# Optimization experiments

Measured on AMD Instinct MI355X. Metric: run time of the kernel, lower is better.

## Reference

```python
import jax, jax.numpy as jnp
import numpy as np

B, T, D, H, Q = 8, 1024, 256, 4, 3
DK = D // H


def _ln(x, g, b):
    m = x.mean(-1, keepdims=True)
    v = x.var(-1, keepdims=True)
    return (x - m) / jnp.sqrt(v + 1e-5) * g + b


def _grn(x, f1w, f1b, f2w, f2b, gw, gb, lng, lnb):
    # GatedResidualNetwork (input_size == output_size, dropout in eval mode)
    eta1 = jax.nn.elu(x @ f1w.T + f1b)
    eta2 = eta1 @ f2w.T + f2b
    a = jax.nn.sigmoid(eta2 @ gw.T + gb) * eta2
    return _ln(x + a, lng, lnb)


def setup_inputs() -> dict:
    key = jax.random.key(0)
    ks = jax.random.split(key, 24)
    s = 0.02
    p = {}
    p['x'] = jax.random.normal(ks[0], (B, T, D), dtype=jnp.float32)
    # GRN 1 (temporal enrichment before attention)
    p['g1_f1w'] = jax.random.normal(ks[1], (D, D)) * s
    p['g1_f1b'] = jnp.zeros((D,))
    p['g1_f2w'] = jax.random.normal(ks[2], (D, D)) * s
    p['g1_f2b'] = jnp.zeros((D,))
    p['g1_gw'] = jax.random.normal(ks[3], (D, D)) * s
    p['g1_gb'] = jnp.zeros((D,))
    p['g1_lng'] = jnp.ones((D,))
    p['g1_lnb'] = jnp.zeros((D,))
    # Multi-head self-attention
    p['wq'] = jax.random.normal(ks[4], (D, D)) * s
    p['wk'] = jax.random.normal(ks[5], (D, D)) * s
    p['wv'] = jax.random.normal(ks[6], (D, D)) * s
    p['wo_w'] = jax.random.normal(ks[7], (D, D)) * s
    p['wo_b'] = jnp.zeros((D,))
    p['attn_lng'] = jnp.ones((D,))
    p['attn_lnb'] = jnp.zeros((D,))
    # GRN 2 (post-attention gating)
    p['g2_f1w'] = jax.random.normal(ks[8], (D, D)) * s
    p['g2_f1b'] = jnp.zeros((D,))
    p['g2_f2w'] = jax.random.normal(ks[9], (D, D)) * s
    p['g2_f2b'] = jnp.zeros((D,))
    p['g2_gw'] = jax.random.normal(ks[10], (D, D)) * s
    p['g2_gb'] = jnp.zeros((D,))
    p['g2_lng'] = jnp.ones((D,))
    p['g2_lnb'] = jnp.zeros((D,))
    # Quantile heads: Linear(D -> Q)
    p['qh_w'] = jax.random.normal(ks[11], (Q, D)) * s
    p['qh_b'] = jnp.zeros((Q,))
    return p


def reference(x, g1_f1w, g1_f1b, g1_f2w, g1_f2b, g1_gw, g1_gb, g1_lng, g1_lnb,
              wq, wk, wv, wo_w, wo_b, attn_lng, attn_lnb,
              g2_f1w, g2_f1b, g2_f2w, g2_f2b, g2_gw, g2_gb, g2_lng, g2_lnb,
              qh_w, qh_b):
    b, t, d = x.shape
    h = _grn(x, g1_f1w, g1_f1b, g1_f2w, g1_f2b, g1_gw, g1_gb, g1_lng, g1_lnb)
    # self-attention (W_q/W_k/W_v have no bias, per module)
    q = (h @ wq.T).reshape(b, t, H, DK)
    k = (h @ wk.T).reshape(b, t, H, DK)
    v = (h @ wv.T).reshape(b, t, H, DK)
    scale = 1.0 / np.sqrt(DK).astype(np.float32)
    scores = jnp.einsum('bthd,bshd->bhts', q, k) * scale  # [B,H,T,T]
    attn = jax.nn.softmax(scores, axis=-1)
    ctx = jnp.einsum('bhts,bshd->bthd', attn, v).reshape(b, t, d)
    attn_out = ctx @ wo_w.T + wo_b
    h2 = _ln(h + attn_out, attn_lng, attn_lnb)
    h3 = _grn(h2, g2_f1w, g2_f1b, g2_f2w, g2_f2b, g2_gw, g2_gb, g2_lng, g2_lnb)
    # quantile heads on the last decoder step (CUDAQuantileHeadsFunction: [B,D]->[B,Q])
    out = h3[:, -1, :] @ qh_w.T + qh_b  # [B, Q]
    return out
```

## Files before the change

### kernel.cpp

```cpp
#include <hip/hip_runtime.h>
#include <hip/hip_bf16.h>
#include <math.h>

#define DD 256
#define BB 8
#define TT 1024
#define MM (BB*TT)
#define NH 4
#define DKH 64
#define NQ 3

typedef __attribute__((ext_vector_type(8))) short bf16x8;
typedef __attribute__((ext_vector_type(4))) float f32x4;
typedef unsigned short u16;
typedef unsigned int u32;

__device__ __forceinline__ float bf2f(u16 u) {
  return __uint_as_float(((u32)u) << 16);
}
__device__ __forceinline__ u16 f2bf(float x) {
  __hip_bfloat16 h = __float2bfloat16(x);
  return *reinterpret_cast<u16*>(&h);
}
__device__ __forceinline__ uint2 pack4(float a, float b, float c, float d) {
  uint2 r;
  r.x = (u32)f2bf(a) | ((u32)f2bf(b) << 16);
  r.y = (u32)f2bf(c) | ((u32)f2bf(d) << 16);
  return r;
}
__device__ __forceinline__ float wred(float v) {
#pragma unroll
  for (int off = 32; off; off >>= 1) v += __shfl_xor(v, off);
  return v;
}

template<bool ABF, int ACT>
__global__ __launch_bounds__(256) void gemm64(const void* __restrict__ A_,
                                              const float* __restrict__ W,
                                              const float* __restrict__ bias,
                                              u16* __restrict__ out)
{
  __shared__ u16 As[64][264];
  __shared__ u16 Bs[64][264];
  const int tid  = threadIdx.x;
  const int lane = tid & 63, wave = tid >> 6;
  const int wr = wave >> 1, wc = wave & 1;
  const int q  = lane >> 4, lr = lane & 15;
  const int m0 = blockIdx.x * 64, n0 = blockIdx.y * 64;

#pragma unroll
  for (int p = 0; p < 8; ++p) {
    const int c = tid + p * 256;
    const int row = c >> 5, col = (c & 31) * 8;
    if constexpr (ABF) {
      *(uint4*)&As[row][col] = *(const uint4*)((const u16*)A_ + (size_t)(m0 + row) * DD + col);
    } else {
      const float* ap = (const float*)A_ + (size_t)(m0 + row) * DD + col;
      const float4 v0 = *(const float4*)ap, v1 = *(const float4*)(ap + 4);
      *(uint2*)&As[row][col]     = pack4(v0.x, v0.y, v0.z, v0.w);
      *(uint2*)&As[row][col + 4] = pack4(v1.x, v1.y, v1.z, v1.w);
    }
    const float* wp = W + (size_t)(n0 + row) * DD + col;
    const float4 w0 = *(const float4*)wp, w1 = *(const float4*)(wp + 4);
    *(uint2*)&Bs[row][col]     = pack4(w0.x, w0.y, w0.z, w0.w);
    *(uint2*)&Bs[row][col + 4] = pack4(w1.x, w1.y, w1.z, w1.w);
  }
  __syncthreads();

  f32x4 acc[2][2] = {};
#pragma unroll
  for (int kk = 0; kk < 8; ++kk) {
    const int koff = kk * 32 + q * 8;
    bf16x8 av[2], bv[2];
    av[0] = *(const bf16x8*)&As[wr * 32 + lr][koff];
    av[1] = *(const bf16x8*)&As[wr * 32 + 16 + lr][koff];
    bv[0] = *(const bf16x8*)&Bs[wc * 32 + lr][koff];
    bv[1] = *(const bf16x8*)&Bs[wc * 32 + 16 + lr][koff];
#pragma unroll
    for (int i = 0; i < 2; ++i)
#pragma unroll
      for (int j = 0; j < 2; ++j)
        acc[i][j] = __builtin_amdgcn_mfma_f32_16x16x32_bf16(av[i], bv[j], acc[i][j], 0, 0, 0);
  }

#pragma unroll
  for (int i = 0; i < 2; ++i) {
#pragma unroll
    for (int j = 0; j < 2; ++j) {
      const int col = n0 + wc * 32 + j * 16 + lr;
      const float bvv = bias ? bias[col] : 0.f;
#pragma unroll
      for (int t = 0; t < 4; ++t) {
        const int row = m0 + wr * 32 + i * 16 + q * 4 + t;
        float v = acc[i][j][t] + bvv;
        if (ACT == 1) v = v > 0.f ? v : expm1f(v);
        out[(size_t)row * DD + col] = f2bf(v);
      }
    }
  }
}

__global__ __launch_bounds__(256) void gemm_kv(const u16* __restrict__ A_,
                                               const float* __restrict__ Wk,
                                               const float* __restrict__ Wv,
                                               u16* __restrict__ kout,
                                               u16* __restrict__ vout)
{
  __shared__ u16 As[64][264];
  __shared__ u16 Bs[64][264];
  const int tid  = threadIdx.x;
  const int lane = tid & 63, wave = tid >> 6;
  const int wr = wave >> 1, wc = wave & 1;
  const int q  = lane >> 4, lr = lane & 15;
  const int ny = blockIdx.y;
  const float* W = (ny < 4) ? Wk : Wv;
  u16* out = (ny < 4) ? kout : vout;
  const int m0 = blockIdx.x * 64, n0 = (ny & 3) * 64;

#pragma unroll
  for (int p = 0; p < 8; ++p) {
    const int c = tid + p * 256;
    const int row = c >> 5, col = (c & 31) * 8;
    *(uint4*)&As[row][col] = *(const uint4*)(A_ + (size_t)(m0 + row) * DD + col);
    const float* wp = W + (size_t)(n0 + row) * DD + col;
    const float4 w0 = *(const float4*)wp, w1 = *(const float4*)(wp + 4);
    *(uint2*)&Bs[row][col]     = pack4(w0.x, w0.y, w0.z, w0.w);
    *(uint2*)&Bs[row][col + 4] = pack4(w1.x, w1.y, w1.z, w1.w);
  }
  __syncthreads();

  f32x4 acc[2][2] = {};
#pragma unroll
  for (int kk = 0; kk < 8; ++kk) {
    const int koff = kk * 32 + q * 8;
    bf16x8 av[2], bv[2];
    av[0] = *(const bf16x8*)&As[wr * 32 + lr][koff];
    av[1] = *(const bf16x8*)&As[wr * 32 + 16 + lr][koff];
    bv[0] = *(const bf16x8*)&Bs[wc * 32 + lr][koff];
    bv[1] = *(const bf16x8*)&Bs[wc * 32 + 16 + lr][koff];
#pragma unroll
    for (int i = 0; i < 2; ++i)
#pragma unroll
      for (int j = 0; j < 2; ++j)
        acc[i][j] = __builtin_amdgcn_mfma_f32_16x16x32_bf16(av[i], bv[j], acc[i][j], 0, 0, 0);
  }

#pragma unroll
  for (int i = 0; i < 2; ++i) {
#pragma unroll
    for (int j = 0; j < 2; ++j) {
      const int col = n0 + wc * 32 + j * 16 + lr;
#pragma unroll
      for (int t = 0; t < 4; ++t) {
        const int row = m0 + wr * 32 + i * 16 + q * 4 + t;
        out[(size_t)row * DD + col] = f2bf(acc[i][j][t]);
      }
    }
  }
}

__global__ __launch_bounds__(256) void grn_gate_ln(
    const u16* __restrict__ eta2, const float* __restrict__ W,
    const float* __restrict__ gb, const float* __restrict__ x,
    const float* __restrict__ lng, const float* __restrict__ lnb,
    u16* __restrict__ hout, float* __restrict__ hlast)
{
  __shared__ u16 As[32][136];
  __shared__ u16 Bs[256][136];
  __shared__ float red_s[32][5];
  __shared__ float red_q[32][5];
  __shared__ float smean[32], srstd[32];

  const int tid  = threadIdx.x;
  const int lane = tid & 63, wave = tid >> 6;
  const int q  = lane >> 4, lr = lane & 15;
  const int m0 = blockIdx.x * 32;

  f32x4 acc[2][4] = {};

  for (int k0 = 0; k0 < DD; k0 += 128) {
#pragma unroll
    for (int p = 0; p < 2; ++p) {
      const int c = tid + p * 256;
      const int row = c >> 4, col = (c & 15) * 8;
      *(uint4*)&As[row][col] = *(const uint4*)(eta2 + (size_t)(m0 + row) * DD + k0 + col);
    }
#pragma unroll
    for (int p = 0; p < 16; ++p) {
      const int c = tid + p * 256;
      const int row = c >> 4, col = (c & 15) * 8;
      const float* wp = W + (size_t)row * DD + k0 + col;
      const float4 w0 = *(const float4*)wp, w1 = *(const float4*)(wp + 4);
      *(uint2*)&Bs[row][col]     = pack4(w0.x, w0.y, w0.z, w0.w);
      *(uint2*)&Bs[row][col + 4] = pack4(w1.x, w1.y, w1.z, w1.w);
    }
    __syncthreads();
#pragma unroll
    for (int kk = 0; kk < 4; ++kk) {
      const int koff = kk * 32 + q * 8;
      bf16x8 av[2], bv[4];
#pragma unroll
      for (int i = 0; i < 2; ++i) av[i] = *(const bf16x8*)&As[i * 16 + lr][koff];
#pragma unroll
      for (int j = 0; j < 4; ++j) bv[j] = *(const bf16x8*)&Bs[wave * 64 + j * 16 + lr][koff];
#pragma unroll
      for (int i = 0; i < 2; ++i)
#pragma unroll
        for (int j = 0; j < 4; ++j)
          acc[i][j] = __builtin_amdgcn_mfma_f32_16x16x32_bf16(av[i], bv[j], acc[i][j], 0, 0, 0);
    }
    __syncthreads();
  }

  float pre[2][4][4];
#pragma unroll
  for (int i = 0; i < 2; ++i) {
#pragma unroll
    for (int j = 0; j < 4; ++j) {
      const int n = wave * 64 + j * 16 + lr;
      const float gbn = gb[n];
#pragma unroll
      for (int t = 0; t < 4; ++t) {
        const int grow = m0 + i * 16 + q * 4 + t;
        const float gate = acc[i][j][t] + gbn;
        const float sig = 1.f / (1.f + expf(-gate));
        const float e2 = bf2f(eta2[(size_t)grow * DD + n]);
        pre[i][j][t] = x[(size_t)grow * DD + n] + sig * e2;
      }
    }
  }
#pragma unroll
  for (int i = 0; i < 2; ++i) {
#pragma unroll
    for (int t = 0; t < 4; ++t) {
      float s = 0.f, sq = 0.f;
#pragma unroll
      for (int j = 0; j < 4; ++j) { const float v = pre[i][j][t]; s += v; sq += v * v; }
#pragma unroll
      for (int m = 1; m <= 8; m <<= 1) { s += __shfl_xor(s, m); sq += __shfl_xor(sq, m); }
      if (lr == 0) {
        const int ml = i * 16 + q * 4 + t;
        red_s[ml][wave] = s;
        red_q[ml][wave] = sq;
      }
    }
  }
  __syncthreads();
  if (tid < 32) {
    const float s  = red_s[tid][0] + red_s[tid][1] + red_s[tid][2] + red_s[tid][3];
    const float sq = red_q[tid][0] + red_q[tid][1] + red_q[tid][2] + red_q[tid][3];
    const float mean = s * (1.f / DD);
    const float var = sq * (1.f / DD) - mean * mean;
    smean[tid] = mean;
    srstd[tid] = rsqrtf(var + 1e-5f);
  }
  __syncthreads();
#pragma unroll
  for (int i = 0; i < 2; ++i) {
#pragma unroll
    for (int j = 0; j < 4; ++j) {
      const int n = wave * 64 + j * 16 + lr;
      const float gn = lng[n], bn = lnb[n];
#pragma unroll
      for (int t = 0; t < 4; ++t) {
        const int ml = i * 16 + q * 4 + t;
        const int grow = m0 + ml;
        const float hn = (pre[i][j][t] - smean[ml]) * srstd[ml] * gn + bn;
        hout[(size_t)grow * DD + n] = f2bf(hn);
        if ((grow & (TT - 1)) == (TT - 1))
          hlast[(size_t)(grow >> 10) * DD + n] = hn;
      }
    }
  }
}

__global__ __launch_bounds__(256) void qk_softmax_ctx(
    const float* __restrict__ hlast, const u16* __restrict__ kbuf,
    const u16* __restrict__ vbuf, const float* __restrict__ wq,
    const float* __restrict__ wow, const float* __restrict__ f1w,
    const float* __restrict__ f2w, const float* __restrict__ gw,
    u16* __restrict__ wbf, float* __restrict__ ctxbuf)
{
  __shared__ float hl[DD], qh[DKH];
  __shared__ float red[8];
  __shared__ float pr[TT];
  __shared__ float part[8][DKH];
  const int h = blockIdx.x, b = blockIdx.y;
  const int tid = threadIdx.x, lane = tid & 63, w = tid >> 6;

  {
    const int bid = b * NH + h;
    const int mi = bid >> 3;
    const float* src = (mi == 0) ? wow : (mi == 1) ? f1w : (mi == 2) ? f2w : gw;
    const int off = (bid & 7) * 8192 + tid * 32;
    const float* sp = src + off;
    u16* dp = wbf + mi * 65536 + off;
#pragma unroll
    for (int i = 0; i < 32; i += 4) {
      const float4 v = *(const float4*)(sp + i);
      *(uint2*)(dp + i) = pack4(v.x, v.y, v.z, v.w);
    }
  }

  hl[tid] = hlast[(size_t)b * DD + tid];
  __syncthreads();
  {
    const int j = tid >> 2, seg = tid & 3;
    const float* wr = wq + (size_t)(h * DKH + j) * DD + seg * 64;
    const float* sp = hl + seg * 64;
    float acc = 0.f;
#pragma unroll
    for (int k = 0; k < 64; k += 4) {
      const float4 w4 = *(const float4*)(wr + k);
      acc += w4.x * sp[k] + w4.y * sp[k + 1] + w4.z * sp[k + 2] + w4.w * sp[k + 3];
    }
    acc += __shfl_xor(acc, 1);
    acc += __shfl_xor(acc, 2);
    if (seg == 0) qh[j] = acc;
  }
  __syncthreads();

  float sv[4], mx = -3.0e38f;
#pragma unroll
  for (int i = 0; i < 4; ++i) {
    const int s = tid + 256 * i;
    const u16* kr = kbuf + ((size_t)(b * TT + s)) * DD + h * DKH;
    float acc = 0.f;
#pragma unroll
    for (int d = 0; d < DKH; d += 8) {
      const bf16x8 kv = *(const bf16x8*)(kr + d);
#pragma unroll
      for (int e = 0; e < 8; ++e) acc += bf2f((u16)kv[e]) * qh[d + e];
    }
    sv[i] = acc * 0.125f;
    mx = fmaxf(mx, sv[i]);
  }
#pragma unroll
  for (int off = 32; off; off >>= 1) mx = fmaxf(mx, __shfl_xor(mx, off));
  if (lane == 0) red[w] = mx;
  __syncthreads();
  mx = fmaxf(fmaxf(red[0], red[1]), fmaxf(red[2], red[3]));
  float sum = 0.f;
#pragma unroll
  for (int i = 0; i < 4; ++i) { sv[i] = expf(sv[i] - mx); sum += sv[i]; }
  sum = wred(sum);
  if (lane == 0) red[4 + w] = sum;
  __syncthreads();
  const float inv = 1.f / (red[4] + red[5] + red[6] + red[7]);
#pragma unroll
  for (int i = 0; i < 4; ++i) pr[tid + 256 * i] = sv[i] * inv;
  __syncthreads();

  {
    const int np = (tid & 31) * 2, sg = tid >> 5;
    const u16* vp = vbuf + ((size_t)(b * TT + sg * 128)) * DD + h * DKH + np;
    const float* pp = pr + sg * 128;
    float a0 = 0.f, a1 = 0.f;
    for (int s = 0; s < 128; ++s) {
      const u32 vv = *(const u32*)(vp + (size_t)s * DD);
      const float p = pp[s];
      a0 += p * bf2f((u16)(vv & 0xffffu));
      a1 += p * bf2f((u16)(vv >> 16));
    }
    part[sg][np] = a0; part[sg][np + 1] = a1;
  }
  __syncthreads();
  if (tid < DKH) {
    float s = 0.f;
#pragma unroll
    for (int g = 0; g < 8; ++g) s += part[g][tid];
    ctxbuf[(size_t)b * DD + h * DKH + tid] = s;
  }
}

__device__ __forceinline__ void mv256b(const u16* __restrict__ W16,
                                       const float* __restrict__ srcbuf,
                                       float* __restrict__ dst,
                                       int wave, int lane)
{
  const int half = lane >> 5, l32 = lane & 31;
  float s[8];
  {
    const float4 s0 = *(const float4*)(srcbuf + l32 * 8);
    const float4 s1 = *(const float4*)(srcbuf + l32 * 8 + 4);
    s[0] = s0.x; s[1] = s0.y; s[2] = s0.z; s[3] = s0.w;
    s[4] = s1.x; s[5] = s1.y; s[6] = s1.z; s[7] = s1.w;
  }
#pragma unroll
  for (int i = 0; i < 8; ++i) {
    const int r = wave * 16 + i * 2 + half;
    const bf16x8 wv = *(const bf16x8*)(W16 + (size_t)r * DD + l32 * 8);
    float acc = 0.f;
#pragma unroll
    for (int e = 0; e < 8; ++e) acc += bf2f((u16)wv[e]) * s[e];
#pragma unroll
    for (int off = 16; off; off >>= 1) acc += __shfl_xor(acc, off);
    if (l32 == 0) dst[r] = acc;
  }
}

#define LN_STEP(val, gam, bet, dst) \
  __syncthreads(); \
  if (tid < DD) { lnS[tid] = (val); lnQ[tid] = (val) * (val); } \
  __syncthreads(); \
  if (tid < 64) { \
    float s_ = 0.f, q_ = 0.f; \
    _Pragma("unroll") \
    for (int i_ = 0; i_ < 4; ++i_) { s_ += lnS[tid + 64 * i_]; q_ += lnQ[tid + 64 * i_]; } \
    s_ = wred(s_); q_ = wred(q_); \
    if (tid == 0) { const float m_ = s_ * (1.f / DD); red2[0] = m_; red2[1] = rsqrtf(q_ * (1.f / DD) - m_ * m_ + 1e-5f); } \
  } \
  __syncthreads(); \
  if (tid < DD) dst[tid] = ((val) - red2[0]) * red2[1] * gam[tid] + bet[tid]; \
  __syncthreads();

__global__ __launch_bounds__(1024) void tail2(
    const float* __restrict__ hlast, const float* __restrict__ ctxbuf,
    const u16* __restrict__ wbf,
    const float* __restrict__ wob, const float* __restrict__ alng, const float* __restrict__ alnb,
    const float* __restrict__ f1b, const float* __restrict__ f2b,
    const float* __restrict__ gbv, const float* __restrict__ lng, const float* __restrict__ lnb,
    const float* __restrict__ qhw, const float* __restrict__ qhb,
    float* __restrict__ out)
{
  __shared__ float hl[DD], bufA[DD], bufB[DD], bufC[DD], part0[DD];
  __shared__ float lnS[DD], lnQ[DD];
  __shared__ float red2[2];
  const int b = blockIdx.x, tid = threadIdx.x;
  const int wave = tid >> 6, lane = tid & 63;

  if (tid < DD) {
    hl[tid]   = hlast[(size_t)b * DD + tid];
    bufB[tid] = ctxbuf[(size_t)b * DD + tid];
  }
  __syncthreads();

  mv256b(wbf + 0 * 65536, bufB, part0, wave, lane);
  __syncthreads();
  float v = 0.f;
  if (tid < DD) v = hl[tid] + part0[tid] + wob[tid];
  LN_STEP(v, alng, alnb, bufA)

  mv256b(wbf + 1 * 65536, bufA, part0, wave, lane);
  __syncthreads();
  if (tid < DD) {
    const float e1 = part0[tid] + f1b[tid];
    bufB[tid] = e1 > 0.f ? e1 : expm1f(e1);
  }
  __syncthreads();

  mv256b(wbf + 2 * 65536, bufB, part0, wave, lane);
  __syncthreads();
  if (tid < DD) bufC[tid] = part0[tid] + f2b[tid];
  __syncthreads();

  mv256b(wbf + 3 * 65536, bufC, part0, wave, lane);
  __syncthreads();
  v = 0.f;
  if (tid < DD) {
    const float g = part0[tid] + gbv[tid];
    v = bufA[tid] + (1.f / (1.f + expf(-g))) * bufC[tid];
  }
  LN_STEP(v, lng, lnb, bufA)

  if (tid < 64 * NQ) {
    const int qi = tid >> 6, l = tid & 63;
    float acc = 0.f;
#pragma unroll
    for (int i = 0; i < 4; ++i) acc += qhw[(size_t)qi * DD + l + 64 * i] * bufA[l + 64 * i];
    acc = wred(acc);
    if (l == 0) out[b * NQ + qi] = acc + qhb[qi];
  }
}

extern "C" void kernel_launch(void* const* d_in, const int* in_sizes, int n_in,
                              void* d_out, int out_size, void* d_ws, size_t ws_size,
                              hipStream_t stream)
{
  const float* x       = (const float*)d_in[0];
  const float* g1_f1w  = (const float*)d_in[1];
  const float* g1_f1b  = (const float*)d_in[2];
  const float* g1_f2w  = (const float*)d_in[3];
  const float* g1_f2b  = (const float*)d_in[4];
  const float* g1_gw   = (const float*)d_in[5];
  const float* g1_gb   = (const float*)d_in[6];
  const float* g1_lng  = (const float*)d_in[7];
  const float* g1_lnb  = (const float*)d_in[8];
  const float* wq      = (const float*)d_in[9];
  const float* wk      = (const float*)d_in[10];
  const float* wv      = (const float*)d_in[11];
  const float* wo_w    = (const float*)d_in[12];
  const float* wo_b    = (const float*)d_in[13];
  const float* attn_lng= (const float*)d_in[14];
  const float* attn_lnb= (const float*)d_in[15];
  const float* g2_f1w  = (const float*)d_in[16];
  const float* g2_f1b  = (const float*)d_in[17];
  const float* g2_f2w  = (const float*)d_in[18];
  const float* g2_f2b  = (const float*)d_in[19];
  const float* g2_gw   = (const float*)d_in[20];
  const float* g2_gb   = (const float*)d_in[21];
  const float* g2_lng  = (const float*)d_in[22];
  const float* g2_lnb  = (const float*)d_in[23];
  const float* qh_w    = (const float*)d_in[24];
  const float* qh_b    = (const float*)d_in[25];
  float* out = (float*)d_out;

  char* w8 = (char*)d_ws;
  u16*  eta1  = (u16*)(w8);
  u16*  wbf   = (u16*)(w8);
  u16*  eta2  = (u16*)(w8 + ((size_t)4  << 20));
  u16*  hbuf  = (u16*)(w8 + ((size_t)8  << 20));
  u16*  kbuf  = (u16*)(w8 + ((size_t)12 << 20));
  u16*  vbuf  = (u16*)(w8 + ((size_t)16 << 20));
  float* hlast = (float*)(w8 + ((size_t)20 << 20));
  float* ctxbuf = (float*)(w8 + ((size_t)20 << 20) + (64 << 10));

  const dim3 blk(256);
  const dim3 g1(MM / 64, DD / 64);

  gemm64<false, 1><<<g1, blk, 0, stream>>>((const void*)x,    g1_f1w, g1_f1b, eta1);
  gemm64<true,  0><<<g1, blk, 0, stream>>>((const void*)eta1, g1_f2w, g1_f2b, eta2);
  grn_gate_ln<<<dim3(MM / 32), blk, 0, stream>>>(eta2, g1_gw, g1_gb, x, g1_lng, g1_lnb, hbuf, hlast);
  gemm_kv<<<dim3(MM / 64, 8), blk, 0, stream>>>(hbuf, wk, wv, kbuf, vbuf);
  qk_softmax_ctx<<<dim3(NH, BB), blk, 0, stream>>>(hlast, kbuf, vbuf, wq,
                                                   wo_w, g2_f1w, g2_f2w, g2_gw,
                                                   wbf, ctxbuf);
  tail2<<<dim3(BB), dim3(1024), 0, stream>>>(hlast, ctxbuf, wbf,
                                             wo_b, attn_lng, attn_lnb,
                                             g2_f1b, g2_f2b, g2_gb, g2_lng, g2_lnb,
                                             qh_w, qh_b, out);
}
```

Before: 77.19 us.

## Precast input and all weights to bf16 in a dedicated kernel before GEMMs

Adds a precast kernel that converts x and nine weight matrices to bf16 once, so GEMM kernels load bf16 tiles directly instead of converting fp32 per block. This removes repeated weight conversions across the many GEMM blocks and the conversion work inside qk_softmax_ctx. In exchange it adds an extra kernel launch and a full read of x in fp32 plus a bf16 write and reread, which adds memory traffic.

Measured after the change: 77.32 us. Within noise of the previous version (+0.2%).

```diff
diff --git a/kernel.cpp b/kernel.cpp
--- a/kernel.cpp
+++ b/kernel.cpp
@@ -34,9 +34,48 @@
   return v;
 }
 
-template<bool ABF, int ACT>
-__global__ __launch_bounds__(256) void gemm64(const void* __restrict__ A_,
-                                              const float* __restrict__ W,
+#define NX8 (MM * DD / 8)
+#define NW8 (65536 / 8)
+#define NCHUNK (NX8 + 9 * NW8)
+
+__global__ __launch_bounds__(256) void precast(
+    const float* __restrict__ x,
+    const float* __restrict__ w0, const float* __restrict__ w1,
+    const float* __restrict__ w2, const float* __restrict__ w3,
+    const float* __restrict__ w4, const float* __restrict__ w5,
+    const float* __restrict__ w6, const float* __restrict__ w7,
+    const float* __restrict__ w8_, u16* __restrict__ wb,
+    u16* __restrict__ xb)
+{
+  const int c = blockIdx.x * 256 + threadIdx.x;
+  if (c >= NCHUNK) return;
+  const float* src;
+  u16* dst;
+  int off;
+  if (c < NX8) {
+    src = x; dst = xb; off = c * 8;
+  } else {
+    const int r = c - NX8;
+    const int mi = r / NW8;
+    off = (r - mi * NW8) * 8;
+    switch (mi) {
+      case 0: src = w0; break; case 1: src = w1; break;
+      case 2: src = w2; break; case 3: src = w3; break;
+      case 4: src = w4; break; case 5: src = w5; break;
+      case 6: src = w6; break; case 7: src = w7; break;
+      default: src = w8_; break;
+    }
+    dst = wb + mi * 65536;
+  }
+  const float4 v0 = *(const float4*)(src + off);
+  const float4 v1 = *(const float4*)(src + off + 4);
+  *(uint2*)(dst + off)     = pack4(v0.x, v0.y, v0.z, v0.w);
+  *(uint2*)(dst + off + 4) = pack4(v1.x, v1.y, v1.z, v1.w);
+}
+
+template<int ACT>
+__global__ __launch_bounds__(256) void gemm64(const u16* __restrict__ A_,
+                                              const u16* __restrict__ W,
                                               const float* __restrict__ bias,
                                               u16* __restrict__ out)
 {
@@ -52,18 +91,8 @@
   for (int p = 0; p < 8; ++p) {
     const int c = tid + p * 256;
     const int row = c >> 5, col = (c & 31) * 8;
-    if constexpr (ABF) {
-      *(uint4*)&As[row][col] = *(const uint4*)((const u16*)A_ + (size_t)(m0 + row) * DD + col);
-    } else {
-      const float* ap = (const float*)A_ + (size_t)(m0 + row) * DD + col;
-      const float4 v0 = *(const float4*)ap, v1 = *(const float4*)(ap + 4);
-      *(uint2*)&As[row][col]     = pack4(v0.x, v0.y, v0.z, v0.w);
-      *(uint2*)&As[row][col + 4] = pack4(v1.x, v1.y, v1.z, v1.w);
-    }
-    const float* wp = W + (size_t)(n0 + row) * DD + col;
-    const float4 w0 = *(const float4*)wp, w1 = *(const float4*)(wp + 4);
-    *(uint2*)&Bs[row][col]     = pack4(w0.x, w0.y, w0.z, w0.w);
-    *(uint2*)&Bs[row][col + 4] = pack4(w1.x, w1.y, w1.z, w1.w);
+    *(uint4*)&As[row][col] = *(const uint4*)(A_ + (size_t)(m0 + row) * DD + col);
+    *(uint4*)&Bs[row][col] = *(const uint4*)(W  + (size_t)(n0 + row) * DD + col);
   }
   __syncthreads();
 
@@ -101,8 +130,8 @@
 }
 
 __global__ __launch_bounds__(256) void gemm_kv(const u16* __restrict__ A_,
-                                               const float* __restrict__ Wk,
-                                               const float* __restrict__ Wv,
+                                               const u16* __restrict__ Wk,
+                                               const u16* __restrict__ Wv,
                                                u16* __restrict__ kout,
                                                u16* __restrict__ vout)
 {
@@ -113,7 +142,7 @@
   const int wr = wave >> 1, wc = wave & 1;
   const int q  = lane >> 4, lr = lane & 15;
   const int ny = blockIdx.y;
-  const float* W = (ny < 4) ? Wk : Wv;
+  const u16* W = (ny < 4) ? Wk : Wv;
   u16* out = (ny < 4) ? kout : vout;
   const int m0 = blockIdx.x * 64, n0 = (ny & 3) * 64;
 
@@ -122,10 +151,7 @@
     const int c = tid + p * 256;
     const int row = c >> 5, col = (c & 31) * 8;
     *(uint4*)&As[row][col] = *(const uint4*)(A_ + (size_t)(m0 + row) * DD + col);
-    const float* wp = W + (size_t)(n0 + row) * DD + col;
-    const float4 w0 = *(const float4*)wp, w1 = *(const float4*)(wp + 4);
-    *(uint2*)&Bs[row][col]     = pack4(w0.x, w0.y, w0.z, w0.w);
-    *(uint2*)&Bs[row][col + 4] = pack4(w1.x, w1.y, w1.z, w1.w);
+    *(uint4*)&Bs[row][col] = *(const uint4*)(W  + (size_t)(n0 + row) * DD + col);
   }
   __syncthreads();
 
@@ -160,7 +186,7 @@
 }
 
 __global__ __launch_bounds__(256) void grn_gate_ln(
-    const u16* __restrict__ eta2, const float* __restrict__ W,
+    const u16* __restrict__ eta2, const u16* __restrict__ W,
     const float* __restrict__ gb, const float* __restrict__ x,
     const float* __restrict__ lng, const float* __restrict__ lnb,
     u16* __restrict__ hout, float* __restrict__ hlast)
@@ -189,10 +215,7 @@
     for (int p = 0; p < 16; ++p) {
       const int c = tid + p * 256;
       const int row = c >> 4, col = (c & 15) * 8;
-      const float* wp = W + (size_t)row * DD + k0 + col;
-      const float4 w0 = *(const float4*)wp, w1 = *(const float4*)(wp + 4);
-      *(uint2*)&Bs[row][col]     = pack4(w0.x, w0.y, w0.z, w0.w);
-      *(uint2*)&Bs[row][col + 4] = pack4(w1.x, w1.y, w1.z, w1.w);
+      *(uint4*)&Bs[row][col] = *(const uint4*)(W + (size_t)row * DD + k0 + col);
     }
     __syncthreads();
 #pragma unroll
@@ -277,9 +300,7 @@
 __global__ __launch_bounds__(256) void qk_softmax_ctx(
     const float* __restrict__ hlast, const u16* __restrict__ kbuf,
     const u16* __restrict__ vbuf, const float* __restrict__ wq,
-    const float* __restrict__ wow, const float* __restrict__ f1w,
-    const float* __restrict__ f2w, const float* __restrict__ gw,
-    u16* __restrict__ wbf, float* __restrict__ ctxbuf)
+    float* __restrict__ ctxbuf)
 {
   __shared__ float hl[DD], qh[DKH];
   __shared__ float red[8];
@@ -287,20 +308,6 @@
   __shared__ float part[8][DKH];
   const int h = blockIdx.x, b = blockIdx.y;
   const int tid = threadIdx.x, lane = tid & 63, w = tid >> 6;
-
-  {
-    const int bid = b * NH + h;
-    const int mi = bid >> 3;
-    const float* src = (mi == 0) ? wow : (mi == 1) ? f1w : (mi == 2) ? f2w : gw;
-    const int off = (bid & 7) * 8192 + tid * 32;
-    const float* sp = src + off;
-    u16* dp = wbf + mi * 65536 + off;
-#pragma unroll
-    for (int i = 0; i < 32; i += 4) {
-      const float4 v = *(const float4*)(sp + i);
-      *(uint2*)(dp + i) = pack4(v.x, v.y, v.z, v.w);
-    }
-  }
 
   hl[tid] = hlast[(size_t)b * DD + tid];
   __syncthreads();
@@ -506,26 +513,29 @@
   float* out = (float*)d_out;
 
   char* w8 = (char*)d_ws;
-  u16*  eta1  = (u16*)(w8);
-  u16*  wbf   = (u16*)(w8);
-  u16*  eta2  = (u16*)(w8 + ((size_t)4  << 20));
-  u16*  hbuf  = (u16*)(w8 + ((size_t)8  << 20));
-  u16*  kbuf  = (u16*)(w8 + ((size_t)12 << 20));
-  u16*  vbuf  = (u16*)(w8 + ((size_t)16 << 20));
-  float* hlast = (float*)(w8 + ((size_t)20 << 20));
-  float* ctxbuf = (float*)(w8 + ((size_t)20 << 20) + (64 << 10));
+  u16*  wb    = (u16*)(w8);
+  u16*  xb    = (u16*)(w8 + ((size_t)2  << 20));
+  u16*  eta1  = (u16*)(w8 + ((size_t)6  << 20));
+  u16*  eta2  = (u16*)(w8 + ((size_t)10 << 20));
+  u16*  hbuf  = (u16*)(w8 + ((size_t)14 << 20));
+  u16*  kbuf  = (u16*)(w8 + ((size_t)18 << 20));
+  u16*  vbuf  = (u16*)(w8 + ((size_t)22 << 20));
+  float* hlast = (float*)(w8 + ((size_t)26 << 20));
+  float* ctxbuf = (float*)(w8 + ((size_t)26 << 20) + (64 << 10));
 
   const dim3 blk(256);
   const dim3 g1(MM / 64, DD / 64);
 
-  gemm64<false, 1><<<g1, blk, 0, stream>>>((const void*)x,    g1_f1w, g1_f1b, eta1);
-  gemm64<true,  0><<<g1, blk, 0, stream>>>((const void*)eta1, g1_f2w, g1_f2b, eta2);
-  grn_gate_ln<<<dim3(MM / 32), blk, 0, stream>>>(eta2, g1_gw, g1_gb, x, g1_lng, g1_lnb, hbuf, hlast);
-  gemm_kv<<<dim3(MM / 64, 8), blk, 0, stream>>>(hbuf, wk, wv, kbuf, vbuf);
-  qk_softmax_ctx<<<dim3(NH, BB), blk, 0, stream>>>(hlast, kbuf, vbuf, wq,
-                                                   wo_w, g2_f1w, g2_f2w, g2_gw,
-                                                   wbf, ctxbuf);
-  tail2<<<dim3(BB), dim3(1024), 0, stream>>>(hlast, ctxbuf, wbf,
+  precast<<<dim3((NCHUNK + 255) / 256), blk, 0, stream>>>(
+      x, g1_f1w, g1_f2w, g1_gw, wk, wv, wo_w, g2_f1w, g2_f2w, g2_gw, wb, xb);
+  gemm64<1><<<g1, blk, 0, stream>>>(xb,   wb + 0 * 65536, g1_f1b, eta1);
+  gemm64<0><<<g1, blk, 0, stream>>>(eta1, wb + 1 * 65536, g1_f2b, eta2);
+  grn_gate_ln<<<dim3(MM / 32), blk, 0, stream>>>(eta2, wb + 2 * 65536, g1_gb, x,
+                                                 g1_lng, g1_lnb, hbuf, hlast);
+  gemm_kv<<<dim3(MM / 64, 8), blk, 0, stream>>>(hbuf, wb + 3 * 65536, wb + 4 * 65536,
+                                                kbuf, vbuf);
+  qk_softmax_ctx<<<dim3(NH, BB), blk, 0, stream>>>(hlast, kbuf, vbuf, wq, ctxbuf);
+  tail2<<<dim3(BB), dim3(1024), 0, stream>>>(hlast, ctxbuf, wb + 5 * 65536,
                                              wo_b, attn_lng, attn_lnb,
                                              g2_f1b, g2_f2b, g2_gb, g2_lng, g2_lnb,
                                              qh_w, qh_b, out);
```

## Fold K/V projections into query-side vectors and split attention over sequence chunks

Applied to the files above, without the earlier changes.

Drops the full K and V GEMMs over all 8192 rows. The last-step query is projected back through Wk, so scores come straight from dot products with h. Unnormalised exp-weighted sums of h are built in 16 chunks per batch, then reduced in the tail and projected through Wv once. This removes the large K/V GEMM and its intermediate buffers and spreads attention over more blocks. In exchange, softmax no longer subtracts a max and instead clamps scores to ±30, which could lose accuracy for large scores.

Measured after the change: 89.60 us. +16.1%, slower.

```diff
diff --git a/kernel.cpp b/kernel.cpp
--- a/kernel.cpp
+++ b/kernel.cpp
@@ -9,6 +9,8 @@
 #define NH 4
 #define DKH 64
 #define NQ 3
+#define SPLIT 16
+#define SROWS (TT/SPLIT)
 
 typedef __attribute__((ext_vector_type(8))) short bf16x8;
 typedef __attribute__((ext_vector_type(4))) float f32x4;
@@ -100,65 +102,6 @@
   }
 }
 
-__global__ __launch_bounds__(256) void gemm_kv(const u16* __restrict__ A_,
-                                               const float* __restrict__ Wk,
-                                               const float* __restrict__ Wv,
-                                               u16* __restrict__ kout,
-                                               u16* __restrict__ vout)
-{
-  __shared__ u16 As[64][264];
-  __shared__ u16 Bs[64][264];
-  const int tid  = threadIdx.x;
-  const int lane = tid & 63, wave = tid >> 6;
-  const int wr = wave >> 1, wc = wave & 1;
-  const int q  = lane >> 4, lr = lane & 15;
-  const int ny = blockIdx.y;
-  const float* W = (ny < 4) ? Wk : Wv;
-  u16* out = (ny < 4) ? kout : vout;
-  const int m0 = blockIdx.x * 64, n0 = (ny & 3) * 64;
-
-#pragma unroll
-  for (int p = 0; p < 8; ++p) {
-    const int c = tid + p * 256;
-    const int row = c >> 5, col = (c & 31) * 8;
-    *(uint4*)&As[row][col] = *(const uint4*)(A_ + (size_t)(m0 + row) * DD + col);
-    const float* wp = W + (size_t)(n0 + row) * DD + col;
-    const float4 w0 = *(const float4*)wp, w1 = *(const float4*)(wp + 4);
-    *(uint2*)&Bs[row][col]     = pack4(w0.x, w0.y, w0.z, w0.w);
-    *(uint2*)&Bs[row][col + 4] = pack4(w1.x, w1.y, w1.z, w1.w);
-  }
-  __syncthreads();
-
-  f32x4 acc[2][2] = {};
-#pragma unroll
-  for (int kk = 0; kk < 8; ++kk) {
-    const int koff = kk * 32 + q * 8;
-    bf16x8 av[2], bv[2];
-    av[0] = *(const bf16x8*)&As[wr * 32 + lr][koff];
-    av[1] = *(const bf16x8*)&As[wr * 32 + 16 + lr][koff];
-    bv[0] = *(const bf16x8*)&Bs[wc * 32 + lr][koff];
-    bv[1] = *(const bf16x8*)&Bs[wc * 32 + 16 + lr][koff];
-#pragma unroll
-    for (int i = 0; i < 2; ++i)
-#pragma unroll
-      for (int j = 0; j < 2; ++j)
-        acc[i][j] = __builtin_amdgcn_mfma_f32_16x16x32_bf16(av[i], bv[j], acc[i][j], 0, 0, 0);
-  }
-
-#pragma unroll
-  for (int i = 0; i < 2; ++i) {
-#pragma unroll
-    for (int j = 0; j < 2; ++j) {
-      const int col = n0 + wc * 32 + j * 16 + lr;
-#pragma unroll
-      for (int t = 0; t < 4; ++t) {
-        const int row = m0 + wr * 32 + i * 16 + q * 4 + t;
-        out[(size_t)row * DD + col] = f2bf(acc[i][j][t]);
-      }
-    }
-  }
-}
-
 __global__ __launch_bounds__(256) void grn_gate_ln(
     const u16* __restrict__ eta2, const float* __restrict__ W,
     const float* __restrict__ gb, const float* __restrict__ x,
@@ -274,102 +217,125 @@
   }
 }
 
-__global__ __launch_bounds__(256) void qk_softmax_ctx(
-    const float* __restrict__ hlast, const u16* __restrict__ kbuf,
-    const u16* __restrict__ vbuf, const float* __restrict__ wq,
-    const float* __restrict__ wow, const float* __restrict__ f1w,
+__global__ __launch_bounds__(256) void attn_partial(
+    const float* __restrict__ hlast, const u16* __restrict__ hbuf,
+    const float* __restrict__ wq, const float* __restrict__ wk,
+    const float* __restrict__ wo_w, const float* __restrict__ f1w,
     const float* __restrict__ f2w, const float* __restrict__ gw,
-    u16* __restrict__ wbf, float* __restrict__ ctxbuf)
+    const float* __restrict__ wv,
+    u16* __restrict__ wbf,
+    float* __restrict__ p_eh,
+    float* __restrict__ p_den)
 {
-  __shared__ float hl[DD], qh[DKH];
-  __shared__ float red[8];
-  __shared__ float pr[TT];
-  __shared__ float part[8][DKH];
-  const int h = blockIdx.x, b = blockIdx.y;
+  __shared__ float hl[DD];
+  __shared__ float qv[DD];
+  __shared__ float qk[NH][DD];
+  __shared__ float ehp[4][NH][DD];
+  __shared__ float denp[4][NH];
+  const int chunk = blockIdx.x, b = blockIdx.y;
   const int tid = threadIdx.x, lane = tid & 63, w = tid >> 6;
-
-  {
-    const int bid = b * NH + h;
-    const int mi = bid >> 3;
-    const float* src = (mi == 0) ? wow : (mi == 1) ? f1w : (mi == 2) ? f2w : gw;
-    const int off = (bid & 7) * 8192 + tid * 32;
-    const float* sp = src + off;
-    u16* dp = wbf + mi * 65536 + off;
-#pragma unroll
-    for (int i = 0; i < 32; i += 4) {
-      const float4 v = *(const float4*)(sp + i);
-      *(uint2*)(dp + i) = pack4(v.x, v.y, v.z, v.w);
-    }
-  }
-
-  hl[tid] = hlast[(size_t)b * DD + tid];
-  __syncthreads();
-  {
-    const int j = tid >> 2, seg = tid & 3;
-    const float* wr = wq + (size_t)(h * DKH + j) * DD + seg * 64;
-    const float* sp = hl + seg * 64;
-    float acc = 0.f;
-#pragma unroll
-    for (int k = 0; k < 64; k += 4) {
-      const float4 w4 = *(const float4*)(wr + k);
-      acc += w4.x * sp[k] + w4.y * sp[k + 1] + w4.z * sp[k + 2] + w4.w * sp[k + 3];
-    }
-    acc += __shfl_xor(acc, 1);
-    acc += __shfl_xor(acc, 2);
-    if (seg == 0) qh[j] = acc;
-  }
-  __syncthreads();
-
-  float sv[4], mx = -3.0e38f;
-#pragma unroll
-  for (int i = 0; i < 4; ++i) {
-    const int s = tid + 256 * i;
-    const u16* kr = kbuf + ((size_t)(b * TT + s)) * DD + h * DKH;
-    float acc = 0.f;
-#pragma unroll
-    for (int d = 0; d < DKH; d += 8) {
-      const bf16x8 kv = *(const bf16x8*)(kr + d);
-#pragma unroll
-      for (int e = 0; e < 8; ++e) acc += bf2f((u16)kv[e]) * qh[d + e];
-    }
-    sv[i] = acc * 0.125f;
-    mx = fmaxf(mx, sv[i]);
-  }
-#pragma unroll
-  for (int off = 32; off; off >>= 1) mx = fmaxf(mx, __shfl_xor(mx, off));
-  if (lane == 0) red[w] = mx;
-  __syncthreads();
-  mx = fmaxf(fmaxf(red[0], red[1]), fmaxf(red[2], red[3]));
-  float sum = 0.f;
-#pragma unroll
-  for (int i = 0; i < 4; ++i) { sv[i] = expf(sv[i] - mx); sum += sv[i]; }
-  sum = wred(sum);
-  if (lane == 0) red[4 + w] = sum;
-  __syncthreads();
-  const float inv = 1.f / (red[4] + red[5] + red[6] + red[7]);
-#pragma unroll
-  for (int i = 0; i < 4; ++i) pr[tid + 256 * i] = sv[i] * inv;
-  __syncthreads();
-
-  {
-    const int np = (tid & 31) * 2, sg = tid >> 5;
-    const u16* vp = vbuf + ((size_t)(b * TT + sg * 128)) * DD + h * DKH + np;
-    const float* pp = pr + sg * 128;
-    float a0 = 0.f, a1 = 0.f;
-    for (int s = 0; s < 128; ++s) {
-      const u32 vv = *(const u32*)(vp + (size_t)s * DD);
-      const float p = pp[s];
-      a0 += p * bf2f((u16)(vv & 0xffffu));
-      a1 += p * bf2f((u16)(vv >> 16));
-    }
-    part[sg][np] = a0; part[sg][np + 1] = a1;
-  }
-  __syncthreads();
-  if (tid < DKH) {
-    float s = 0.f;
-#pragma unroll
-    for (int g = 0; g < 8; ++g) s += part[g][tid];
-    ctxbuf[(size_t)b * DD + h * DKH + tid] = s;
+  const int l32 = lane & 31, half = lane >> 5;
+
+  {
+    const int bid = b * SPLIT + chunk;
+    const int base = bid * 2560;
+#pragma unroll
+    for (int r = 0; r < 10; ++r) {
+      const int e = base + r * 256 + tid;
+      const int mi = e >> 16, off = e & 65535;
+      const float* s = (mi == 0) ? wo_w : (mi == 1) ? f1w : (mi == 2) ? f2w
+                     : (mi == 3) ? gw : wv;
+      wbf[e] = f2bf(s[off]);
+    }
+  }
+
+  if (tid < DD) hl[tid] = hlast[(size_t)b * DD + tid];
+  __syncthreads();
+
+  {
+    float sv[8];
+    const float4 s0 = *(const float4*)(hl + l32 * 8);
+    const float4 s1 = *(const float4*)(hl + l32 * 8 + 4);
+    sv[0] = s0.x; sv[1] = s0.y; sv[2] = s0.z; sv[3] = s0.w;
+    sv[4] = s1.x; sv[5] = s1.y; sv[6] = s1.z; sv[7] = s1.w;
+#pragma unroll
+    for (int i = 0; i < 32; ++i) {
+      const int r = w * 64 + i * 2 + half;
+      const float* wr_ = wq + (size_t)r * DD + l32 * 8;
+      const float4 w0 = *(const float4*)wr_;
+      const float4 w1 = *(const float4*)(wr_ + 4);
+      float acc = w0.x * sv[0] + w0.y * sv[1] + w0.z * sv[2] + w0.w * sv[3]
+                + w1.x * sv[4] + w1.y * sv[5] + w1.z * sv[6] + w1.w * sv[7];
+#pragma unroll
+      for (int off = 16; off; off >>= 1) acc += __shfl_xor(acc, off);
+      if (l32 == 0) qv[r] = acc;
+    }
+  }
+  __syncthreads();
+
+  {
+    float acc[4] = {};
+    for (int d = 0; d < 64; ++d) {
+      const int r = w * 64 + d;
+      const float qd = qv[r];
+      const float4 kv = *(const float4*)(wk + (size_t)r * DD + lane * 4);
+      acc[0] += qd * kv.x; acc[1] += qd * kv.y;
+      acc[2] += qd * kv.z; acc[3] += qd * kv.w;
+    }
+#pragma unroll
+    for (int i = 0; i < 4; ++i) qk[w][lane * 4 + i] = acc[i] * 0.125f;
+  }
+  __syncthreads();
+
+  {
+    float qkr[NH][4];
+#pragma unroll
+    for (int h = 0; h < NH; ++h) {
+      const float4 qq = *(const float4*)&qk[h][lane * 4];
+      qkr[h][0] = qq.x; qkr[h][1] = qq.y; qkr[h][2] = qq.z; qkr[h][3] = qq.w;
+    }
+    float ehacc[NH][4] = {};
+    float dacc[NH] = {};
+    const int sbase = chunk * SROWS + w * 16;
+    for (int ii = 0; ii < 16; ++ii) {
+      const int s = sbase + ii;
+      const uint2 hv2 = *(const uint2*)(hbuf + ((size_t)(b * TT + s)) * DD + lane * 4);
+      float hv[4];
+      hv[0] = bf2f((u16)(hv2.x & 0xffffu)); hv[1] = bf2f((u16)(hv2.x >> 16));
+      hv[2] = bf2f((u16)(hv2.y & 0xffffu)); hv[3] = bf2f((u16)(hv2.y >> 16));
+      float sc[NH];
+#pragma unroll
+      for (int h = 0; h < NH; ++h) {
+        float p = qkr[h][0] * hv[0] + qkr[h][1] * hv[1]
+                + qkr[h][2] * hv[2] + qkr[h][3] * hv[3];
+        sc[h] = wred(p);
+      }
+#pragma unroll
+      for (int h = 0; h < NH; ++h) {
+        const float E = __expf(fminf(fmaxf(sc[h], -30.f), 30.f));
+        dacc[h] += E;
+        ehacc[h][0] += E * hv[0]; ehacc[h][1] += E * hv[1];
+        ehacc[h][2] += E * hv[2]; ehacc[h][3] += E * hv[3];
+      }
+    }
+#pragma unroll
+    for (int h = 0; h < NH; ++h) {
+      *(float4*)&ehp[w][h][lane * 4] =
+          make_float4(ehacc[h][0], ehacc[h][1], ehacc[h][2], ehacc[h][3]);
+      if (lane == 0) denp[w][h] = dacc[h];
+    }
+  }
+  __syncthreads();
+
+  {
+    const size_t pb = ((size_t)(b * SPLIT + chunk)) * NH * DD;
+#pragma unroll
+    for (int h = 0; h < NH; ++h)
+      p_eh[pb + h * DD + tid] =
+          ehp[0][h][tid] + ehp[1][h][tid] + ehp[2][h][tid] + ehp[3][h][tid];
+    if (tid < NH)
+      p_den[(b * SPLIT + chunk) * NH + tid] =
+          denp[0][tid] + denp[1][tid] + denp[2][tid] + denp[3][tid];
   }
 }
 
@@ -414,24 +380,54 @@
   if (tid < DD) dst[tid] = ((val) - red2[0]) * red2[1] * gam[tid] + bet[tid]; \
   __syncthreads();
 
-__global__ __launch_bounds__(1024) void tail2(
-    const float* __restrict__ hlast, const float* __restrict__ ctxbuf,
-    const u16* __restrict__ wbf,
+__global__ __launch_bounds__(1024) void tail3(
+    const float* __restrict__ hlast, const float* __restrict__ p_eh,
+    const float* __restrict__ p_den, const u16* __restrict__ wbf,
     const float* __restrict__ wob, const float* __restrict__ alng, const float* __restrict__ alnb,
     const float* __restrict__ f1b, const float* __restrict__ f2b,
     const float* __restrict__ gbv, const float* __restrict__ lng, const float* __restrict__ lnb,
     const float* __restrict__ qhw, const float* __restrict__ qhb,
     float* __restrict__ out)
 {
+  __shared__ float pv[NH * DD];
+  __shared__ float den[NH];
   __shared__ float hl[DD], bufA[DD], bufB[DD], bufC[DD], part0[DD];
   __shared__ float lnS[DD], lnQ[DD];
   __shared__ float red2[2];
   const int b = blockIdx.x, tid = threadIdx.x;
   const int wave = tid >> 6, lane = tid & 63;
-
-  if (tid < DD) {
-    hl[tid]   = hlast[(size_t)b * DD + tid];
-    bufB[tid] = ctxbuf[(size_t)b * DD + tid];
+  const int half = lane >> 5, l32 = lane & 31;
+
+  float ehsum = 0.f;
+  for (int c = 0; c < SPLIT; ++c)
+    ehsum += p_eh[((size_t)(b * SPLIT + c)) * NH * DD + tid];
+  if (tid < NH) {
+    float s = 0.f;
+    for (int c = 0; c < SPLIT; ++c) s += p_den[(b * SPLIT + c) * NH + tid];
+    den[tid] = s;
+  }
+  if (tid < DD) hl[tid] = hlast[(size_t)b * DD + tid];
+  __syncthreads();
+  pv[tid] = ehsum / den[tid >> 8];
+  __syncthreads();
+
+  {
+    const u16* wv16 = wbf + 4 * 65536;
+#pragma unroll
+    for (int i = 0; i < 8; ++i) {
+      const int r = wave * 16 + i * 2 + half;
+      const float* sp = pv + (r >> 6) * DD + l32 * 8;
+      const float4 s0 = *(const float4*)sp;
+      const float4 s1 = *(const float4*)(sp + 4);
+      const bf16x8 wvv = *(const bf16x8*)(wv16 + (size_t)r * DD + l32 * 8);
+      float acc = bf2f((u16)wvv[0]) * s0.x + bf2f((u16)wvv[1]) * s0.y
+                + bf2f((u16)wvv[2]) * s0.z + bf2f((u16)wvv[3]) * s0.w
+                + bf2f((u16)wvv[4]) * s1.x + bf2f((u16)wvv[5]) * s1.y
+                + bf2f((u16)wvv[6]) * s1.z + bf2f((u16)wvv[7]) * s1.w;
+#pragma unroll
+      for (int off = 16; off; off >>= 1) acc += __shfl_xor(acc, off);
+      if (l32 == 0) bufB[r] = acc;
+    }
   }
   __syncthreads();
 
@@ -506,14 +502,13 @@
   float* out = (float*)d_out;
 
   char* w8 = (char*)d_ws;
-  u16*  eta1  = (u16*)(w8);
   u16*  wbf   = (u16*)(w8);
-  u16*  eta2  = (u16*)(w8 + ((size_t)4  << 20));
-  u16*  hbuf  = (u16*)(w8 + ((size_t)8  << 20));
-  u16*  kbuf  = (u16*)(w8 + ((size_t)12 << 20));
-  u16*  vbuf  = (u16*)(w8 + ((size_t)16 << 20));
-  float* hlast = (float*)(w8 + ((size_t)20 << 20));
-  float* ctxbuf = (float*)(w8 + ((size_t)20 << 20) + (64 << 10));
+  float* p_eh  = (float*)(w8 + ((size_t)1 << 20));
+  float* p_den = (float*)(w8 + ((size_t)1600 << 10));
+  u16*  eta1  = (u16*)(w8 + ((size_t)2  << 20));
+  u16*  eta2  = (u16*)(w8 + ((size_t)6  << 20));
+  u16*  hbuf  = (u16*)(w8 + ((size_t)10 << 20));
+  float* hlast = (float*)(w8 + ((size_t)14 << 20));
 
   const dim3 blk(256);
   const dim3 g1(MM / 64, DD / 64);
@@ -521,11 +516,10 @@
   gemm64<false, 1><<<g1, blk, 0, stream>>>((const void*)x,    g1_f1w, g1_f1b, eta1);
   gemm64<true,  0><<<g1, blk, 0, stream>>>((const void*)eta1, g1_f2w, g1_f2b, eta2);
   grn_gate_ln<<<dim3(MM / 32), blk, 0, stream>>>(eta2, g1_gw, g1_gb, x, g1_lng, g1_lnb, hbuf, hlast);
-  gemm_kv<<<dim3(MM / 64, 8), blk, 0, stream>>>(hbuf, wk, wv, kbuf, vbuf);
-  qk_softmax_ctx<<<dim3(NH, BB), blk, 0, stream>>>(hlast, kbuf, vbuf, wq,
-                                                   wo_w, g2_f1w, g2_f2w, g2_gw,
-                                                   wbf, ctxbuf);
-  tail2<<<dim3(BB), dim3(1024), 0, stream>>>(hlast, ctxbuf, wbf,
+  attn_partial<<<dim3(SPLIT, BB), blk, 0, stream>>>(hlast, hbuf, wq, wk,
+                                                    wo_w, g2_f1w, g2_f2w, g2_gw, wv,
+                                                    wbf, p_eh, p_den);
+  tail3<<<dim3(BB), dim3(1024), 0, stream>>>(hlast, p_eh, p_den, wbf,
                                              wo_b, attn_lng, attn_lnb,
                                              g2_f1b, g2_f2b, g2_gb, g2_lng, g2_lnb,
                                              qh_w, qh_b, out);
```
